# Optimization experiments

Measured on AMD Instinct MI355X. Metric: run time of the kernel, lower is better.

## Reference

```python
import jax, jax.numpy as jnp
import numpy as np

ALPHA = 0.2  # LeakyReLU negative slope

def setup_inputs() -> dict:
    key = jax.random.key(0)
    k1, k2, k3 = jax.random.split(key, 3)
    B, N, D_in, D_out = 4, 512, 512, 256
    H = jax.random.normal(k1, (B, N, D_in), dtype=jnp.float32)
    # xavier-style scaled params
    W = jax.random.normal(k2, (D_out, D_in), dtype=jnp.float32) * (2.0 / (D_in + D_out)) ** 0.5
    a = jax.random.normal(k3, (D_out, 1), dtype=jnp.float32) * (2.0 / (D_out + 1)) ** 0.5
    return {"H": H, "W": W, "a": a}

def reference(H, W, a):
    # Wh: [B, N, D_out]
    Wh = jnp.einsum('bnd,od->bno', H, W)
    # additive pairwise scores: e[b,i,j] = leakyrelu(Wh[b,i]+Wh[b,j]) . a
    e = jnp.einsum('bijo,o->bij',
                   jax.nn.leaky_relu(Wh[:, :, None, :] + Wh[:, None, :, :], ALPHA),
                   a[:, 0])
    attention = jax.nn.softmax(e, axis=-1)          # [B, N, N]
    H_att = jnp.einsum('bij,bjo->bio', attention, Wh)  # [B, N, D_out]
    return H_att
```

## Files before the change

### kernel.cpp

```cpp
#include <hip/hip_runtime.h>

constexpr int Bq   = 4;
constexpr int Nq   = 512;
constexpr int DIN  = 512;
constexpr int DOUT = 256;

typedef float v2f __attribute__((ext_vector_type(2)));
typedef float v4f __attribute__((ext_vector_type(4)));

__device__ __forceinline__ v4f fma4v(const float s, const v4f v, const v4f acc) {
    v4f sv = s;
    return __builtin_elementwise_fma(sv, v, acc);
}

__global__ __launch_bounds__(256) void k0_wt(const float* __restrict__ W,
                                             float* __restrict__ WT) {
    __shared__ float tile[32][33];
    const int k0 = blockIdx.x * 32;
    const int o0 = blockIdx.y * 32;
    const int tx = threadIdx.x;
    const int ty = threadIdx.y;
#pragma unroll
    for (int j = 0; j < 4; ++j)
        tile[ty + 8 * j][tx] = W[(o0 + ty + 8 * j) * DIN + k0 + tx];
    __syncthreads();
#pragma unroll
    for (int j = 0; j < 4; ++j)
        WT[(k0 + ty + 8 * j) * DOUT + o0 + tx] = tile[tx][ty + 8 * j];
}

__global__ __launch_bounds__(512, 4) void k1_wh(const float* __restrict__ H,
                                                const float* __restrict__ WT,
                                                const float* __restrict__ a,
                                                float* __restrict__ Wh,
                                                float* __restrict__ WhT,
                                                float* __restrict__ r) {
    const int t   = threadIdx.x;
    const int blk = blockIdx.x;
    const int b   = blk & 3;
    const int n0  = (blk >> 2) << 2;
    const int p   = __builtin_amdgcn_readfirstlane(t >> 6);
    const int oq  = t & 63;

    __shared__ float sH[4 * 512];
    __shared__ v4f   sPart[8][4][64];

    {
        const v4f* src = (const v4f*)(H + ((size_t)(b * Nq) + n0) * DIN);
        ((v4f*)sH)[t] = src[t];
    }
    __syncthreads();

    const v4f* __restrict__ wt4 = (const v4f*)WT + oq;

    v4f acc[4];
#pragma unroll
    for (int rr = 0; rr < 4; ++rr) acc[rr] = (v4f)0.f;

    const int k0 = p * 64;
    v4f bufA[4], bufB[4];
#pragma unroll
    for (int s = 0; s < 4; ++s) bufA[s] = wt4[(k0 + s) * 64];

    for (int it = 0; it < 8; ++it) {
        const int kA = k0 + it * 8, kB = kA + 4;
#pragma unroll
        for (int s = 0; s < 4; ++s) bufB[s] = wt4[(kB + s) * 64];
#pragma unroll
        for (int rr = 0; rr < 4; ++rr) {
            const v4f h4 = *(const v4f*)&sH[rr * 512 + kA];
            acc[rr] = fma4v(h4.x, bufA[0], acc[rr]);
            acc[rr] = fma4v(h4.y, bufA[1], acc[rr]);
            acc[rr] = fma4v(h4.z, bufA[2], acc[rr]);
            acc[rr] = fma4v(h4.w, bufA[3], acc[rr]);
        }
        if (it < 7) {
#pragma unroll
            for (int s = 0; s < 4; ++s) bufA[s] = wt4[(kA + 8 + s) * 64];
        }
#pragma unroll
        for (int rr = 0; rr < 4; ++rr) {
            const v4f h4 = *(const v4f*)&sH[rr * 512 + kB];
            acc[rr] = fma4v(h4.x, bufB[0], acc[rr]);
            acc[rr] = fma4v(h4.y, bufB[1], acc[rr]);
            acc[rr] = fma4v(h4.z, bufB[2], acc[rr]);
            acc[rr] = fma4v(h4.w, bufB[3], acc[rr]);
        }
    }

#pragma unroll
    for (int rr = 0; rr < 4; ++rr) sPart[p][rr][oq] = acc[rr];
    __syncthreads();

    if (p < 4) {
        const int g = p;
        v4f fin = (v4f)0.f;
#pragma unroll
        for (int pp = 0; pp < 8; ++pp) fin += sPart[pp][g][oq];

        ((v4f*)(Wh + ((size_t)(b * Nq) + n0 + g) * DOUT))[oq] = fin;

        float* wT = WhT + (size_t)b * DOUT * Nq;
        wT[(4 * oq + 0) * Nq + n0 + g] = fin.x;
        wT[(4 * oq + 1) * Nq + n0 + g] = fin.y;
        wT[(4 * oq + 2) * Nq + n0 + g] = fin.z;
        wT[(4 * oq + 3) * Nq + n0 + g] = fin.w;

        const v4f a4 = ((const v4f*)a)[oq];
        float rp = a4.x * fin.x + a4.y * fin.y + a4.z * fin.z + a4.w * fin.w;
#pragma unroll
        for (int off = 32; off > 0; off >>= 1) rp += __shfl_xor(rp, off);
        if ((t & 63) == 0) r[(size_t)b * Nq + n0 + g] = rp;
    }
}

__global__ __launch_bounds__(1024, 4) void k23(const float* __restrict__ Wh,
                                               const float* __restrict__ WhT,
                                               const float* __restrict__ a,
                                               const float* __restrict__ r,
                                               float* __restrict__ out) {
    const int t   = threadIdx.x;
    const int blk = blockIdx.x;
    const int b   = blk & 3;
    const int i0  = (blk >> 2) << 3;

    __shared__ float smem[8192];
    __shared__ float sP[8 * 512];
    __shared__ float wred[2][8][4];

    {
        const int q  = __builtin_amdgcn_readfirstlane(t >> 8);
        const int jp = t & 255;
        const int obase = q * 64;

        const v2f* __restrict__ wj2 =
            (const v2f*)(WhT + (size_t)b * DOUT * Nq + (size_t)obase * Nq) + jp;
        const float* __restrict__ gwi = Wh + ((size_t)b * Nq + i0) * DOUT;
        const float* __restrict__ gr  = r + (size_t)b * Nq;

        v2f ab[8];
#pragma unroll
        for (int rr = 0; rr < 8; ++rr) ab[rr] = (v2f)0.f;
        v2f bufA[8], bufB[8];

#pragma unroll
        for (int s = 0; s < 8; ++s) bufA[s] = wj2[s * 256];

        for (int cc = 0; cc < 4; ++cc) {
            const int oA = cc * 16, oB = oA + 8;
#pragma unroll
            for (int s = 0; s < 8; ++s) bufB[s] = wj2[(oB + s) * 256];
#pragma unroll
            for (int gg = 0; gg < 2; ++gg) {
                const int o4 = obase + oA + gg * 4;
                const float4 a4 = *(const float4*)(a + o4);
#pragma unroll
                for (int rr = 0; rr < 8; ++rr) {
                    const float4 wi4 = *(const float4*)(gwi + rr * DOUT + o4);
#pragma unroll
                    for (int s2 = 0; s2 < 4; ++s2) {
                        const float aq = ((const float*)&a4)[s2];
                        const float wi = ((const float*)&wi4)[s2];
                        v2f w  = bufA[gg * 4 + s2] + wi;
                        v2f aw = __builtin_elementwise_max(w, -w);
                        v2f av = aq;
                        ab[rr] = __builtin_elementwise_fma(av, aw, ab[rr]);
                    }
                }
            }
            if (cc < 3) {
#pragma unroll
                for (int s = 0; s < 8; ++s) bufA[s] = wj2[(oA + 16 + s) * 256];
            }
#pragma unroll
            for (int gg = 0; gg < 2; ++gg) {
                const int o4 = obase + oB + gg * 4;
                const float4 a4 = *(const float4*)(a + o4);
#pragma unroll
                for (int rr = 0; rr < 8; ++rr) {
                    const float4 wi4 = *(const float4*)(gwi + rr * DOUT + o4);
#pragma unroll
                    for (int s2 = 0; s2 < 4; ++s2) {
                        const float aq = ((const float*)&a4)[s2];
                        const float wi = ((const float*)&wi4)[s2];
                        v2f w  = bufB[gg * 4 + s2] + wi;
                        v2f aw = __builtin_elementwise_max(w, -w);
                        v2f av = aq;
                        ab[rr] = __builtin_elementwise_fma(av, aw, ab[rr]);
                    }
                }
            }
        }

        v2f* sAb = (v2f*)smem;
        if (q >= 2) {
#pragma unroll
            for (int rr = 0; rr < 8; ++rr) sAb[((q - 2) * 8 + rr) * 256 + jp] = ab[rr];
        }
        __syncthreads();
        if (q < 2) {
#pragma unroll
            for (int rr = 0; rr < 8; ++rr) ab[rr] += sAb[(q * 8 + rr) * 256 + jp];
        }
        __syncthreads();
        if (q == 1) {
#pragma unroll
            for (int rr = 0; rr < 8; ++rr) sAb[(0 * 8 + rr) * 256 + jp] = ab[rr];
        }
        __syncthreads();

        float e0[8], e1[8];
        if (q == 0) {
            const v2f rj2 = ((const v2f*)gr)[jp];
#pragma unroll
            for (int rr = 0; rr < 8; ++rr) {
                const v2f x = sAb[(0 * 8 + rr) * 256 + jp];
                const float A0 = ab[rr].x + x.x;
                const float A1 = ab[rr].y + x.y;
                const float ri = gr[i0 + rr];
                e0[rr] = 0.6f * (ri + rj2.x) + 0.4f * A0;
                e1[rr] = 0.6f * (ri + rj2.y) + 0.4f * A1;
            }
        }

        const int lane = t & 63;
        const int w    = (t >> 6) & 3;

#pragma unroll
        for (int rr = 0; rr < 8; ++rr) {
            float v = (q == 0) ? fmaxf(e0[rr], e1[rr]) : -3e38f;
#pragma unroll
            for (int off = 32; off > 0; off >>= 1) v = fmaxf(v, __shfl_xor(v, off));
            if (lane == 0 && q == 0) wred[0][rr][w] = v;
        }
        __syncthreads();

        float p0[8], p1[8];
        if (q == 0) {
#pragma unroll
            for (int rr = 0; rr < 8; ++rr) {
                const float4 qv = *(const float4*)&wred[0][rr][0];
                const float m = fmaxf(fmaxf(qv.x, qv.y), fmaxf(qv.z, qv.w));
                p0[rr] = __expf(e0[rr] - m);
                p1[rr] = __expf(e1[rr] - m);
            }
        }
#pragma unroll
        for (int rr = 0; rr < 8; ++rr) {
            float v = (q == 0) ? (p0[rr] + p1[rr]) : 0.f;
#pragma unroll
            for (int off = 32; off > 0; off >>= 1) v += __shfl_xor(v, off);
            if (lane == 0 && q == 0) wred[1][rr][w] = v;
        }
        __syncthreads();

        if (q == 0) {
#pragma unroll
            for (int rr = 0; rr < 8; ++rr) {
                const float4 qv = *(const float4*)&wred[1][rr][0];
                const float inv = 1.0f / (qv.x + qv.y + qv.z + qv.w);
                ((v2f*)sP)[rr * 256 + jp] = (v2f){p0[rr] * inv, p1[rr] * inv};
            }
        }
        __syncthreads();
    }

    {
        const int p2 = __builtin_amdgcn_readfirstlane(t >> 6);
        const int jh = p2 & 7;
        const int rh = p2 >> 3;
        const int oq = t & 63;

        const v4f* __restrict__ wh4 = (const v4f*)(Wh + (size_t)b * Nq * DOUT) + oq;

        v4f acc[4];
#pragma unroll
        for (int rr = 0; rr < 4; ++rr) acc[rr] = (v4f)0.f;

        const int j0 = jh * 64;
        v4f bufA[4], bufB[4];
#pragma unroll
        for (int s = 0; s < 4; ++s) bufA[s] = wh4[(j0 + s) * 64];

        for (int it = 0; it < 8; ++it) {
            const int jA = j0 + it * 8, jB = jA + 4;
#pragma unroll
            for (int s = 0; s < 4; ++s) bufB[s] = wh4[(jB + s) * 64];
#pragma unroll
            for (int rr = 0; rr < 4; ++rr) {
                const v4f p4 = *(const v4f*)&sP[(rh * 4 + rr) * 512 + jA];
                acc[rr] = fma4v(p4.x, bufA[0], acc[rr]);
                acc[rr] = fma4v(p4.y, bufA[1], acc[rr]);
                acc[rr] = fma4v(p4.z, bufA[2], acc[rr]);
                acc[rr] = fma4v(p4.w, bufA[3], acc[rr]);
            }
            if (it < 7) {
#pragma unroll
                for (int s = 0; s < 4; ++s) bufA[s] = wh4[(jA + 8 + s) * 64];
            }
#pragma unroll
            for (int rr = 0; rr < 4; ++rr) {
                const v4f p4 = *(const v4f*)&sP[(rh * 4 + rr) * 512 + jB];
                acc[rr] = fma4v(p4.x, bufB[0], acc[rr]);
                acc[rr] = fma4v(p4.y, bufB[1], acc[rr]);
                acc[rr] = fma4v(p4.z, bufB[2], acc[rr]);
                acc[rr] = fma4v(p4.w, bufB[3], acc[rr]);
            }
        }

        v4f* sPart = (v4f*)smem;
        if (jh < 4) {
#pragma unroll
            for (int rr = 0; rr < 4; ++rr)
                sPart[(jh * 8 + rh * 4 + rr) * 64 + oq] = acc[rr];
        }
        __syncthreads();
        if (jh >= 4) {
#pragma unroll
            for (int rr = 0; rr < 4; ++rr)
                sPart[((jh - 4) * 8 + rh * 4 + rr) * 64 + oq] += acc[rr];
        }
        __syncthreads();

        if (p2 < 8) {
            const int row = p2;
            v4f fin = sPart[(0 * 8 + row) * 64 + oq] + sPart[(1 * 8 + row) * 64 + oq]
                    + sPart[(2 * 8 + row) * 64 + oq] + sPart[(3 * 8 + row) * 64 + oq];
            ((v4f*)(out + ((size_t)(b * Nq) + i0 + row) * DOUT))[oq] = fin;
        }
    }
}

extern "C" void kernel_launch(void* const* d_in, const int* in_sizes, int n_in,
                              void* d_out, int out_size, void* d_ws, size_t ws_size,
                              hipStream_t stream) {
    const float* H = (const float*)d_in[0];
    const float* W = (const float*)d_in[1];
    const float* a = (const float*)d_in[2];
    float* out = (float*)d_out;

    float* Wh  = (float*)d_ws;
    float* WhT = Wh  + Bq * Nq * DOUT;
    float* r   = WhT + Bq * Nq * DOUT;
    float* WT  = r   + Bq * Nq;

    hipLaunchKernelGGL(k0_wt, dim3(16, 8), dim3(32, 8), 0, stream, W, WT);
    hipLaunchKernelGGL(k1_wh, dim3(512),   dim3(512),   0, stream, H, WT, a, Wh, WhT, r);
    hipLaunchKernelGGL(k23,   dim3(256),   dim3(1024),  0, stream, Wh, WhT, a, r, out);
}
```

Measured before the change: 115.5 us.

## Widen k1 to 1024 threads and deepen register prefetch in k1 and score loop

k1 now uses 1024 threads, with each thread computing 2 output columns (float2) instead of 4. This doubles the wave count to hide global-load latency, at the cost of a partial-sum layout change in the reduction. Both k1's GEMM loop and k23's pairwise score loop switch to 16-deep double-buffered register prefetch with fully unrolled load and compute stages. The vector-extension types are replaced with scalar fmaf and fabsf on float2/float4, which may change codegen, including the use of packed FMA. The deeper buffers raise register pressure.

```diff
diff --git a/kernel.cpp b/kernel.cpp
--- a/kernel.cpp
+++ b/kernel.cpp
@@ -5,12 +5,11 @@
 constexpr int DIN  = 512;
 constexpr int DOUT = 256;
 
-typedef float v2f __attribute__((ext_vector_type(2)));
-typedef float v4f __attribute__((ext_vector_type(4)));
-
-__device__ __forceinline__ v4f fma4v(const float s, const v4f v, const v4f acc) {
-    v4f sv = s;
-    return __builtin_elementwise_fma(sv, v, acc);
+__device__ __forceinline__ void fma4(float4& acc, const float s, const float4 v) {
+    acc.x = __builtin_fmaf(s, v.x, acc.x);
+    acc.y = __builtin_fmaf(s, v.y, acc.y);
+    acc.z = __builtin_fmaf(s, v.z, acc.z);
+    acc.w = __builtin_fmaf(s, v.w, acc.w);
 }
 
 __global__ __launch_bounds__(256) void k0_wt(const float* __restrict__ W,
@@ -29,76 +28,81 @@
         WT[(k0 + ty + 8 * j) * DOUT + o0 + tx] = tile[tx][ty + 8 * j];
 }
 
-__global__ __launch_bounds__(512, 4) void k1_wh(const float* __restrict__ H,
-                                                const float* __restrict__ WT,
-                                                const float* __restrict__ a,
-                                                float* __restrict__ Wh,
-                                                float* __restrict__ WhT,
-                                                float* __restrict__ r) {
+__global__ __launch_bounds__(1024, 4) void k1_wh(const float* __restrict__ H,
+                                                 const float* __restrict__ WT,
+                                                 const float* __restrict__ a,
+                                                 float* __restrict__ Wh,
+                                                 float* __restrict__ WhT,
+                                                 float* __restrict__ r) {
     const int t   = threadIdx.x;
     const int blk = blockIdx.x;
     const int b   = blk & 3;
     const int n0  = (blk >> 2) << 2;
-    const int p   = __builtin_amdgcn_readfirstlane(t >> 6);
-    const int oq  = t & 63;
-
-    __shared__ float sH[4 * 512];
-    __shared__ v4f   sPart[8][4][64];
-
-    {
-        const v4f* src = (const v4f*)(H + ((size_t)(b * Nq) + n0) * DIN);
-        ((v4f*)sH)[t] = src[t];
+    const int p   = __builtin_amdgcn_readfirstlane(t >> 7);
+    const int od  = t & 127;
+
+    __shared__ float  sH[4 * 512];
+    __shared__ float2 sPart[8][4][128];
+
+    if (t < 512) {
+        const float4* src = (const float4*)(H + ((size_t)(b * Nq) + n0) * DIN);
+        ((float4*)sH)[t] = src[t];
     }
     __syncthreads();
 
-    const v4f* __restrict__ wt4 = (const v4f*)WT + oq;
-
-    v4f acc[4];
-#pragma unroll
-    for (int rr = 0; rr < 4; ++rr) acc[rr] = (v4f)0.f;
+    const float2* __restrict__ wt2 = (const float2*)WT + od;
+
+    float2 acc[4];
+#pragma unroll
+    for (int rr = 0; rr < 4; ++rr) acc[rr] = make_float2(0.f, 0.f);
 
     const int k0 = p * 64;
-    v4f bufA[4], bufB[4];
-#pragma unroll
-    for (int s = 0; s < 4; ++s) bufA[s] = wt4[(k0 + s) * 64];
-
-    for (int it = 0; it < 8; ++it) {
-        const int kA = k0 + it * 8, kB = kA + 4;
-#pragma unroll
-        for (int s = 0; s < 4; ++s) bufB[s] = wt4[(kB + s) * 64];
-#pragma unroll
-        for (int rr = 0; rr < 4; ++rr) {
-            const v4f h4 = *(const v4f*)&sH[rr * 512 + kA];
-            acc[rr] = fma4v(h4.x, bufA[0], acc[rr]);
-            acc[rr] = fma4v(h4.y, bufA[1], acc[rr]);
-            acc[rr] = fma4v(h4.z, bufA[2], acc[rr]);
-            acc[rr] = fma4v(h4.w, bufA[3], acc[rr]);
-        }
-        if (it < 7) {
-#pragma unroll
-            for (int s = 0; s < 4; ++s) bufA[s] = wt4[(kA + 8 + s) * 64];
-        }
-#pragma unroll
-        for (int rr = 0; rr < 4; ++rr) {
-            const v4f h4 = *(const v4f*)&sH[rr * 512 + kB];
-            acc[rr] = fma4v(h4.x, bufB[0], acc[rr]);
-            acc[rr] = fma4v(h4.y, bufB[1], acc[rr]);
-            acc[rr] = fma4v(h4.z, bufB[2], acc[rr]);
-            acc[rr] = fma4v(h4.w, bufB[3], acc[rr]);
-        }
-    }
-
-#pragma unroll
-    for (int rr = 0; rr < 4; ++rr) sPart[p][rr][oq] = acc[rr];
+    float2 cA[16], cB[16];
+
+#define K1_LOAD16(buf, kb)                                                  \
+    _Pragma("unroll") for (int s = 0; s < 16; ++s) buf[s] = wt2[((kb) + s) * 128];
+
+#define K1_COMP16(buf, kb)                                                  \
+    _Pragma("unroll") for (int kq = 0; kq < 4; ++kq) {                      \
+        _Pragma("unroll") for (int rr = 0; rr < 4; ++rr) {                  \
+            const float4 h4 = *(const float4*)&sH[rr * 512 + (kb) + kq * 4];\
+            _Pragma("unroll") for (int x = 0; x < 4; ++x) {                 \
+                const float hk = ((const float*)&h4)[x];                    \
+                const float2 wv = buf[kq * 4 + x];                          \
+                acc[rr].x = __builtin_fmaf(hk, wv.x, acc[rr].x);            \
+                acc[rr].y = __builtin_fmaf(hk, wv.y, acc[rr].y);            \
+            }                                                               \
+        }                                                                   \
+    }
+
+    K1_LOAD16(cA, k0)
+    K1_LOAD16(cB, k0 + 16)
+    K1_COMP16(cA, k0)
+    K1_LOAD16(cA, k0 + 32)
+    K1_COMP16(cB, k0 + 16)
+    K1_LOAD16(cB, k0 + 48)
+    K1_COMP16(cA, k0 + 32)
+    K1_COMP16(cB, k0 + 48)
+#undef K1_LOAD16
+#undef K1_COMP16
+
+#pragma unroll
+    for (int rr = 0; rr < 4; ++rr) sPart[p][rr][od] = acc[rr];
     __syncthreads();
 
-    if (p < 4) {
-        const int g = p;
-        v4f fin = (v4f)0.f;
-#pragma unroll
-        for (int pp = 0; pp < 8; ++pp) fin += sPart[pp][g][oq];
-
-        ((v4f*)(Wh + ((size_t)(b * Nq) + n0 + g) * DOUT))[oq] = fin;
+    const int w = __builtin_amdgcn_readfirstlane(t >> 6);
+    if (w < 4) {
+        const int g  = w;
+        const int oq = t & 63;
+        float4 fin = make_float4(0.f, 0.f, 0.f, 0.f);
+#pragma unroll
+        for (int pp = 0; pp < 8; ++pp) {
+            const float2 u = sPart[pp][g][2 * oq];
+            const float2 v = sPart[pp][g][2 * oq + 1];
+            fin.x += u.x; fin.y += u.y; fin.z += v.x; fin.w += v.y;
+        }
+
+        ((float4*)(Wh + ((size_t)(b * Nq) + n0 + g) * DOUT))[oq] = fin;
 
         float* wT = WhT + (size_t)b * DOUT * Nq;
         wT[(4 * oq + 0) * Nq + n0 + g] = fin.x;
@@ -106,7 +110,7 @@
         wT[(4 * oq + 2) * Nq + n0 + g] = fin.z;
         wT[(4 * oq + 3) * Nq + n0 + g] = fin.w;
 
-        const v4f a4 = ((const v4f*)a)[oq];
+        const float4 a4 = ((const float4*)a)[oq];
         float rp = a4.x * fin.x + a4.y * fin.y + a4.z * fin.z + a4.w * fin.w;
 #pragma unroll
         for (int off = 32; off > 0; off >>= 1) rp += __shfl_xor(rp, off);
@@ -133,66 +137,47 @@
         const int jp = t & 255;
         const int obase = q * 64;
 
-        const v2f* __restrict__ wj2 =
-            (const v2f*)(WhT + (size_t)b * DOUT * Nq + (size_t)obase * Nq) + jp;
+        const float2* __restrict__ wj2 =
+            (const float2*)(WhT + (size_t)b * DOUT * Nq + (size_t)obase * Nq) + jp;
         const float* __restrict__ gwi = Wh + ((size_t)b * Nq + i0) * DOUT;
         const float* __restrict__ gr  = r + (size_t)b * Nq;
 
-        v2f ab[8];
-#pragma unroll
-        for (int rr = 0; rr < 8; ++rr) ab[rr] = (v2f)0.f;
-        v2f bufA[8], bufB[8];
-
-#pragma unroll
-        for (int s = 0; s < 8; ++s) bufA[s] = wj2[s * 256];
-
-        for (int cc = 0; cc < 4; ++cc) {
-            const int oA = cc * 16, oB = oA + 8;
-#pragma unroll
-            for (int s = 0; s < 8; ++s) bufB[s] = wj2[(oB + s) * 256];
-#pragma unroll
-            for (int gg = 0; gg < 2; ++gg) {
-                const int o4 = obase + oA + gg * 4;
-                const float4 a4 = *(const float4*)(a + o4);
-#pragma unroll
-                for (int rr = 0; rr < 8; ++rr) {
-                    const float4 wi4 = *(const float4*)(gwi + rr * DOUT + o4);
-#pragma unroll
-                    for (int s2 = 0; s2 < 4; ++s2) {
-                        const float aq = ((const float*)&a4)[s2];
-                        const float wi = ((const float*)&wi4)[s2];
-                        v2f w  = bufA[gg * 4 + s2] + wi;
-                        v2f aw = __builtin_elementwise_max(w, -w);
-                        v2f av = aq;
-                        ab[rr] = __builtin_elementwise_fma(av, aw, ab[rr]);
-                    }
-                }
-            }
-            if (cc < 3) {
-#pragma unroll
-                for (int s = 0; s < 8; ++s) bufA[s] = wj2[(oA + 16 + s) * 256];
-            }
-#pragma unroll
-            for (int gg = 0; gg < 2; ++gg) {
-                const int o4 = obase + oB + gg * 4;
-                const float4 a4 = *(const float4*)(a + o4);
-#pragma unroll
-                for (int rr = 0; rr < 8; ++rr) {
-                    const float4 wi4 = *(const float4*)(gwi + rr * DOUT + o4);
-#pragma unroll
-                    for (int s2 = 0; s2 < 4; ++s2) {
-                        const float aq = ((const float*)&a4)[s2];
-                        const float wi = ((const float*)&wi4)[s2];
-                        v2f w  = bufB[gg * 4 + s2] + wi;
-                        v2f aw = __builtin_elementwise_max(w, -w);
-                        v2f av = aq;
-                        ab[rr] = __builtin_elementwise_fma(av, aw, ab[rr]);
-                    }
-                }
-            }
-        }
-
-        v2f* sAb = (v2f*)smem;
+        float2 ab[8];
+#pragma unroll
+        for (int rr = 0; rr < 8; ++rr) ab[rr] = make_float2(0.f, 0.f);
+        float2 cA[16], cB[16];
+
+#define K2_LOAD16(buf, ob)                                                  \
+    _Pragma("unroll") for (int s = 0; s < 16; ++s) buf[s] = wj2[((ob) + s) * 256];
+
+#define K2_COMP16(buf, ob)                                                  \
+    _Pragma("unroll") for (int og = 0; og < 4; ++og) {                      \
+        const int o4 = obase + (ob) + og * 4;                               \
+        const float4 a4 = *(const float4*)(a + o4);               \
+        _Pragma("unroll") for (int rr = 0; rr < 8; ++rr) {                  \
+            const float4 wi4 = *(const float4*)(gwi + rr * DOUT + o4);      \
+            _Pragma("unroll") for (int x = 0; x < 4; ++x) {                 \
+                const float aq = ((const float*)&a4)[x];                    \
+                const float wi = ((const float*)&wi4)[x];                   \
+                const float2 wv = buf[og * 4 + x];                          \
+                ab[rr].x = __builtin_fmaf(aq, __builtin_fabsf(wi + wv.x), ab[rr].x); \
+                ab[rr].y = __builtin_fmaf(aq, __builtin_fabsf(wi + wv.y), ab[rr].y); \
+            }                                                               \
+        }                                                                   \
+    }
+
+        K2_LOAD16(cA, 0)
+        K2_LOAD16(cB, 16)
+        K2_COMP16(cA, 0)
+        K2_LOAD16(cA, 32)
+        K2_COMP16(cB, 16)
+        K2_LOAD16(cB, 48)
+        K2_COMP16(cA, 32)
+        K2_COMP16(cB, 48)
+#undef K2_LOAD16
+#undef K2_COMP16
+
+        float2* sAb = (float2*)smem;
         if (q >= 2) {
 #pragma unroll
             for (int rr = 0; rr < 8; ++rr) sAb[((q - 2) * 8 + rr) * 256 + jp] = ab[rr];
@@ -200,7 +185,10 @@
         __syncthreads();
         if (q < 2) {
 #pragma unroll
-            for (int rr = 0; rr < 8; ++rr) ab[rr] += sAb[(q * 8 + rr) * 256 + jp];
+            for (int rr = 0; rr < 8; ++rr) {
+                const float2 x = sAb[(q * 8 + rr) * 256 + jp];
+                ab[rr].x += x.x; ab[rr].y += x.y;
+            }
         }
         __syncthreads();
         if (q == 1) {
@@ -211,10 +199,10 @@
 
         float e0[8], e1[8];
         if (q == 0) {
-            const v2f rj2 = ((const v2f*)gr)[jp];
+            const float2 rj2 = ((const float2*)gr)[jp];
 #pragma unroll
             for (int rr = 0; rr < 8; ++rr) {
-                const v2f x = sAb[(0 * 8 + rr) * 256 + jp];
+                const float2 x = sAb[(0 * 8 + rr) * 256 + jp];
                 const float A0 = ab[rr].x + x.x;
                 const float A1 = ab[rr].y + x.y;
                 const float ri = gr[i0 + rr];
@@ -259,7 +247,7 @@
             for (int rr = 0; rr < 8; ++rr) {
                 const float4 qv = *(const float4*)&wred[1][rr][0];
                 const float inv = 1.0f / (qv.x + qv.y + qv.z + qv.w);
-                ((v2f*)sP)[rr * 256 + jp] = (v2f){p0[rr] * inv, p1[rr] * inv};
+                ((float2*)sP)[rr * 256 + jp] = make_float2(p0[rr] * inv, p1[rr] * inv);
             }
         }
         __syncthreads();
@@ -271,14 +259,14 @@
         const int rh = p2 >> 3;
         const int oq = t & 63;
 
-        const v4f* __restrict__ wh4 = (const v4f*)(Wh + (size_t)b * Nq * DOUT) + oq;
-
-        v4f acc[4];
-#pragma unroll
-        for (int rr = 0; rr < 4; ++rr) acc[rr] = (v4f)0.f;
+        const float4* __restrict__ wh4 = (const float4*)(Wh + (size_t)b * Nq * DOUT) + oq;
+
+        float4 acc[4];
+#pragma unroll
+        for (int rr = 0; rr < 4; ++rr) acc[rr] = make_float4(0.f, 0.f, 0.f, 0.f);
 
         const int j0 = jh * 64;
-        v4f bufA[4], bufB[4];
+        float4 bufA[4], bufB[4];
 #pragma unroll
         for (int s = 0; s < 4; ++s) bufA[s] = wh4[(j0 + s) * 64];
 
@@ -288,11 +276,9 @@
             for (int s = 0; s < 4; ++s) bufB[s] = wh4[(jB + s) * 64];
 #pragma unroll
             for (int rr = 0; rr < 4; ++rr) {
-                const v4f p4 = *(const v4f*)&sP[(rh * 4 + rr) * 512 + jA];
-                acc[rr] = fma4v(p4.x, bufA[0], acc[rr]);
-                acc[rr] = fma4v(p4.y, bufA[1], acc[rr]);
-                acc[rr] = fma4v(p4.z, bufA[2], acc[rr]);
-                acc[rr] = fma4v(p4.w, bufA[3], acc[rr]);
+                const float4 p4 = *(const float4*)&sP[(rh * 4 + rr) * 512 + jA];
+                fma4(acc[rr], p4.x, bufA[0]); fma4(acc[rr], p4.y, bufA[1]);
+                fma4(acc[rr], p4.z, bufA[2]); fma4(acc[rr], p4.w, bufA[3]);
             }
             if (it < 7) {
 #pragma unroll
@@ -300,15 +286,13 @@
             }
 #pragma unroll
             for (int rr = 0; rr < 4; ++rr) {
-                const v4f p4 = *(const v4f*)&sP[(rh * 4 + rr) * 512 + jB];
-                acc[rr] = fma4v(p4.x, bufB[0], acc[rr]);
-                acc[rr] = fma4v(p4.y, bufB[1], acc[rr]);
-                acc[rr] = fma4v(p4.z, bufB[2], acc[rr]);
-                acc[rr] = fma4v(p4.w, bufB[3], acc[rr]);
-            }
-        }
-
-        v4f* sPart = (v4f*)smem;
+                const float4 p4 = *(const float4*)&sP[(rh * 4 + rr) * 512 + jB];
+                fma4(acc[rr], p4.x, bufB[0]); fma4(acc[rr], p4.y, bufB[1]);
+                fma4(acc[rr], p4.z, bufB[2]); fma4(acc[rr], p4.w, bufB[3]);
+            }
+        }
+
+        float4* sPart = (float4*)smem;
         if (jh < 4) {
 #pragma unroll
             for (int rr = 0; rr < 4; ++rr)
@@ -317,16 +301,26 @@
         __syncthreads();
         if (jh >= 4) {
 #pragma unroll
-            for (int rr = 0; rr < 4; ++rr)
-                sPart[((jh - 4) * 8 + rh * 4 + rr) * 64 + oq] += acc[rr];
+            for (int rr = 0; rr < 4; ++rr) {
+                float4* d = &sPart[((jh - 4) * 8 + rh * 4 + rr) * 64 + oq];
+                d->x += acc[rr].x; d->y += acc[rr].y;
+                d->z += acc[rr].z; d->w += acc[rr].w;
+            }
         }
         __syncthreads();
 
         if (p2 < 8) {
             const int row = p2;
-            v4f fin = sPart[(0 * 8 + row) * 64 + oq] + sPart[(1 * 8 + row) * 64 + oq]
-                    + sPart[(2 * 8 + row) * 64 + oq] + sPart[(3 * 8 + row) * 64 + oq];
-            ((v4f*)(out + ((size_t)(b * Nq) + i0 + row) * DOUT))[oq] = fin;
+            const float4 f0 = sPart[(0 * 8 + row) * 64 + oq];
+            const float4 f1 = sPart[(1 * 8 + row) * 64 + oq];
+            const float4 f2 = sPart[(2 * 8 + row) * 64 + oq];
+            const float4 f3 = sPart[(3 * 8 + row) * 64 + oq];
+            float4 fin;
+            fin.x = f0.x + f1.x + f2.x + f3.x;
+            fin.y = f0.y + f1.y + f2.y + f3.y;
+            fin.z = f0.z + f1.z + f2.z + f3.z;
+            fin.w = f0.w + f1.w + f2.w + f3.w;
+            ((float4*)(out + ((size_t)(b * Nq) + i0 + row) * DOUT))[oq] = fin;
         }
     }
 }
@@ -345,6 +339,6 @@
     float* WT  = r   + Bq * Nq;
 
     hipLaunchKernelGGL(k0_wt, dim3(16, 8), dim3(32, 8), 0, stream, W, WT);
-    hipLaunchKernelGGL(k1_wh, dim3(512),   dim3(512),   0, stream, H, WT, a, Wh, WhT, r);
-    hipLaunchKernelGGL(k23,   dim3(256),   dim3(1024),  0, stream, Wh, WhT, a, r, out);
-}
+    hipLaunchKernelGGL(k1_wh, dim3(512),   dim3(1024), 0, stream, H, WT, a, Wh, WhT, r);
+    hipLaunchKernelGGL(k23,   dim3(256),   dim3(1024), 0, stream, Wh, WhT, a, r, out);
+}
```

After: 120.6 us. +4.4%, slower.
